# Kernel optimization log

Measured on AMD Instinct MI355X. Metric: run time of the kernel, lower is better.

## Reference

```python
import jax, jax.numpy as jnp
import numpy as np

N = 50000   # num nodes
E = 600000  # num edges (avg degree 12)
IN = 128
OUT = 128


def setup_inputs() -> dict:
    key = jax.random.key(0)
    ks = jax.random.split(key, 6)
    x = jax.random.normal(ks[0], (N, IN), dtype=jnp.float32)
    edge_index = jax.random.randint(ks[1], (2, E), 0, N, dtype=jnp.int32)
    # glorot-ish scaling for the linear weights
    W1 = jax.random.normal(ks[2], (IN, OUT), dtype=jnp.float32) / np.float32(np.sqrt(IN))
    b1 = jnp.zeros((OUT,), dtype=jnp.float32)
    W2 = jax.random.normal(ks[3], (OUT, OUT), dtype=jnp.float32) / np.float32(np.sqrt(OUT))
    b2 = jnp.zeros((OUT,), dtype=jnp.float32)
    return {"x": x, "edge_index": edge_index, "W1": W1, "b1": b1, "W2": W2, "b2": b2}


def gcn_conv(x, src, dst, W, b):
    # PyG GCNConv defaults: add self-loops, symmetric normalization D^-1/2 A D^-1/2.
    n = x.shape[0]
    deg = jax.ops.segment_sum(jnp.ones_like(dst, dtype=x.dtype), dst, num_segments=n)
    dinv = jnp.where(deg > 0, jax.lax.rsqrt(deg), 0.0)
    norm = dinv[src] * dinv[dst]            # [E+N]
    h = x @ W                               # [N, OUT]
    msg = h[src] * norm[:, None]            # gather + scale
    out = jax.ops.segment_sum(msg, dst, num_segments=n)  # scatter-add
    return out + b


def reference(x, edge_index, W1, b1, W2, b2):
    loop = jnp.arange(N, dtype=edge_index.dtype)
    src = jnp.concatenate([edge_index[0], loop])  # self-loops appended
    dst = jnp.concatenate([edge_index[1], loop])
    h = jax.nn.relu(gcn_conv(x, src, dst, W1, b1))
    out = jax.nn.relu(gcn_conv(h, src, dst, W2, b2))
    return out
```

## Files before the change

### kernel.cpp

```cpp
#include <hip/hip_runtime.h>
#include <hip/hip_bf16.h>


#define CAP 64

typedef short s16x8 __attribute__((ext_vector_type(8)));
typedef float f32x4 __attribute__((ext_vector_type(4)));

__device__ __forceinline__ unsigned short bf16_rne(float f) {
    unsigned u = __float_as_uint(f);
    return (unsigned short)((u + 0x7fffu + ((u >> 16) & 1u)) >> 16);
}


__global__ void setup_k(const float* __restrict__ W1, const float* __restrict__ W2,
                        short* __restrict__ wh1, short* __restrict__ wl1,
                        short* __restrict__ wh2, short* __restrict__ wl2,
                        int* __restrict__ cursor, int n) {
    int b = blockIdx.x;
    if (b >= 128) {
        int i = (b - 128) * 1024 + threadIdx.x * 4;
        if (i < n) {
            int4 z = make_int4(0, 0, 0, 0);
            if (i + 4 <= n) *(int4*)(cursor + i) = z;
            else for (int j = i; j < n; ++j) cursor[j] = 0;
        }
        return;
    }
    int gid = b * 256 + threadIdx.x;
    int which = gid >> 14;
    int tid = gid & 16383;
    const float* W = which ? W2 : W1;
    short* wh = which ? wh2 : wh1;
    short* wl = which ? wl2 : wl1;
    int k = tid >> 7, nn = tid & 127;
    float w = W[tid];
    unsigned u = __float_as_uint(w);
    unsigned hibits = (u + 0x7fffu + ((u >> 16) & 1u)) & 0xffff0000u;
    float rem = w - __uint_as_float(hibits);
    int kt = k >> 5, kr = k & 31, nt = nn >> 4, nr = nn & 15;
    int l = ((kr >> 3) << 4) | nr;
    int j = kr & 7;
    int dest = ((kt * 8 + nt) * 64 + l) * 8 + j;
    wh[dest] = (short)(hibits >> 16);
    wl[dest] = (short)bf16_rne(rem);
}

__global__ void fill_k(const int* __restrict__ src, const int* __restrict__ dst,
                       int* __restrict__ cursor, int* __restrict__ adj, int E) {
    int e = blockIdx.x * 256 + threadIdx.x;
    if (e < E) {
        int d = dst[e];
        int p = atomicAdd(&cursor[d], 1);
        if (p < CAP) adj[(size_t)d * CAP + p] = src[e];
    }
}

__device__ __forceinline__ void gemm_tile_compute(const char* lds,
                                                  const s16x8 BH[4][2], const s16x8 BL[4][2],
                                                  const int* __restrict__ cursor,
                                                  unsigned short* __restrict__ Hb,
                                                  int base, int n, int w, int rl, int kg) {
#pragma unroll
    for (int rt = 0; rt < 4; ++rt) {
        int row_local = rt * 16 + rl;
        int arow_byte = row_local * 256;
        int aswz = (row_local & 7) << 4;
        f32x4 acc[2] = {(f32x4){0.f,0.f,0.f,0.f}, (f32x4){0.f,0.f,0.f,0.f}};
#pragma unroll
        for (int kt = 0; kt < 4; ++kt) {
            int coff = (kt * 64 + (kg << 4)) ^ aswz;
            s16x8 ah = *(const s16x8*)(lds + arow_byte + coff);
#pragma unroll
            for (int i = 0; i < 2; ++i) {
                acc[i] = __builtin_amdgcn_mfma_f32_16x16x32_bf16(ah, BH[kt][i], acc[i], 0, 0, 0);
                acc[i] = __builtin_amdgcn_mfma_f32_16x16x32_bf16(ah, BL[kt][i], acc[i], 0, 0, 0);
            }
        }
        int r0 = base + rt * 16 + (kg << 2);
        float d0 = (r0 + 0 < n) ? rsqrtf((float)(cursor[r0 + 0] + 1)) : 0.f;
        float d1 = (r0 + 1 < n) ? rsqrtf((float)(cursor[r0 + 1] + 1)) : 0.f;
        float d2 = (r0 + 2 < n) ? rsqrtf((float)(cursor[r0 + 2] + 1)) : 0.f;
        float d3 = (r0 + 3 < n) ? rsqrtf((float)(cursor[r0 + 3] + 1)) : 0.f;
#pragma unroll
        for (int i = 0; i < 2; ++i) {
            int col = ((w * 2 + i) << 4) | rl;
            if (r0 + 0 < n) Hb[(size_t)(r0 + 0) * 128 + col] = bf16_rne(acc[i][0] * d0);
            if (r0 + 1 < n) Hb[(size_t)(r0 + 1) * 128 + col] = bf16_rne(acc[i][1] * d1);
            if (r0 + 2 < n) Hb[(size_t)(r0 + 2) * 128 + col] = bf16_rne(acc[i][2] * d2);
            if (r0 + 3 < n) Hb[(size_t)(r0 + 3) * 128 + col] = bf16_rne(acc[i][3] * d3);
        }
    }
}

__global__ __launch_bounds__(256) void gemm_mfma_f32(const float* __restrict__ X,
                                                     const short* __restrict__ wbh,
                                                     const short* __restrict__ wbl,
                                                     const int* __restrict__ cursor,
                                                     unsigned short* __restrict__ Hb,
                                                     int n) {
    __shared__ char lds[16384];
    int tid = threadIdx.x;
    int w = tid >> 6;
    int l = tid & 63;
    int rl = l & 15;
    int kg = l >> 4;
    int base = blockIdx.x * 64;

    const s16x8* bh8 = (const s16x8*)wbh;
    const s16x8* bl8 = (const s16x8*)wbl;
    s16x8 BH[4][2], BL[4][2];
#pragma unroll
    for (int kt = 0; kt < 4; ++kt)
#pragma unroll
        for (int i = 0; i < 2; ++i) {
            int f = kt * 8 + (w * 2 + i);
            BH[kt][i] = bh8[f * 64 + l];
            BL[kt][i] = bl8[f * 64 + l];
        }

#pragma unroll
    for (int u = 0; u < 4; ++u) {
        int idx = u * 256 + tid;
        int r = idx >> 4;
        int c0 = (idx & 15) * 8;
        int row = base + r;
        float v[8];
        if (row < n) {
            const float4* p = (const float4*)(X + (size_t)row * 128 + c0);
            float4 a = p[0], b = p[1];
            v[0]=a.x; v[1]=a.y; v[2]=a.z; v[3]=a.w;
            v[4]=b.x; v[5]=b.y; v[6]=b.z; v[7]=b.w;
        } else {
#pragma unroll
            for (int i = 0; i < 8; ++i) v[i] = 0.f;
        }
        short hi8[8];
#pragma unroll
        for (int i = 0; i < 8; ++i) hi8[i] = (short)bf16_rne(v[i]);
        int boff = r * 256 + ((c0 * 2) ^ ((r & 7) << 4));
        *(s16x8*)(lds + boff) = *(const s16x8*)hi8;
    }
    __syncthreads();
    gemm_tile_compute(lds, BH, BL, cursor, Hb, base, n, w, rl, kg);
}

__global__ __launch_bounds__(256) void gemm_mfma_bf16(const unsigned short* __restrict__ T,
                                                      const short* __restrict__ wbh,
                                                      const short* __restrict__ wbl,
                                                      const int* __restrict__ cursor,
                                                      unsigned short* __restrict__ Hb,
                                                      int n) {
    __shared__ char lds[16384];
    int tid = threadIdx.x;
    int w = tid >> 6;
    int l = tid & 63;
    int rl = l & 15;
    int kg = l >> 4;
    int base = blockIdx.x * 64;

    const s16x8* bh8 = (const s16x8*)wbh;
    const s16x8* bl8 = (const s16x8*)wbl;
    s16x8 BH[4][2], BL[4][2];
#pragma unroll
    for (int kt = 0; kt < 4; ++kt)
#pragma unroll
        for (int i = 0; i < 2; ++i) {
            int f = kt * 8 + (w * 2 + i);
            BH[kt][i] = bh8[f * 64 + l];
            BL[kt][i] = bl8[f * 64 + l];
        }

#pragma unroll
    for (int u = 0; u < 4; ++u) {
        int idx = u * 256 + tid;
        int r = idx >> 4;
        int cb = (idx & 15) * 16;
        int row = base + r;
        s16x8 val = {0,0,0,0,0,0,0,0};
        if (row < n) val = *(const s16x8*)(T + (size_t)row * 128 + cb / 2);
        int boff = r * 256 + (cb ^ ((r & 7) << 4));
        *(s16x8*)(lds + boff) = val;
    }
    __syncthreads();
    gemm_tile_compute(lds, BH, BL, cursor, Hb, base, n, w, rl, kg);
}


template <int SPLIT>
__global__ __launch_bounds__(256) void agg_k(const unsigned short* __restrict__ Hs,
                                             const int* __restrict__ cursor,
                                             const int* __restrict__ adj,
                                             const float* __restrict__ bias,
                                             float* __restrict__ fout,
                                             unsigned short* __restrict__ th,
                                             int n) {
    int node = blockIdx.x * 4 + (threadIdx.x >> 6);
    if (node >= n) return;
    node = __builtin_amdgcn_readfirstlane(node);
    int lane = threadIdx.x & 63;

    const unsigned* H1 = (const unsigned*)Hs;
    unsigned sraw = H1[(size_t)node * 64 + lane];
    float ax = __uint_as_float((sraw & 0xffffu) << 16);
    float ay = __uint_as_float(sraw & 0xffff0000u);

    int deg_raw = cursor[node];
    int e1 = deg_raw > CAP ? CAP : deg_raw;
    const int* alist = adj + (size_t)node * CAP;
    int e = 0;

    for (; e + 16 <= e1; e += 16) {
        int s[16];
#pragma unroll
        for (int i = 0; i < 16; ++i) s[i] = alist[e + i];
        unsigned rv[16];
#pragma unroll
        for (int i = 0; i < 16; ++i) rv[i] = H1[(size_t)s[i] * 64 + lane];
#pragma unroll
        for (int i = 0; i < 16; ++i) {
            ax += __uint_as_float((rv[i] & 0xffffu) << 16);
            ay += __uint_as_float(rv[i] & 0xffff0000u);
        }
    }
    for (; e + 4 <= e1; e += 4) {
        int s[4];
#pragma unroll
        for (int i = 0; i < 4; ++i) s[i] = alist[e + i];
        unsigned rv[4];
#pragma unroll
        for (int i = 0; i < 4; ++i) rv[i] = H1[(size_t)s[i] * 64 + lane];
#pragma unroll
        for (int i = 0; i < 4; ++i) {
            ax += __uint_as_float((rv[i] & 0xffffu) << 16);
            ay += __uint_as_float(rv[i] & 0xffff0000u);
        }
    }
    for (; e < e1; ++e) {
        unsigned rv = H1[(size_t)alist[e] * 64 + lane];
        ax += __uint_as_float((rv & 0xffffu) << 16);
        ay += __uint_as_float(rv & 0xffff0000u);
    }

    float di = rsqrtf((float)(deg_raw + 1));
    float2 b = ((const float2*)bias)[lane];
    float a0 = fmaxf(fmaf(ax, di, b.x), 0.f);
    float a1 = fmaxf(fmaf(ay, di, b.y), 0.f);
    if (SPLIT) {
        ((ushort2*)th)[(size_t)node * 64 + lane] = make_ushort2(bf16_rne(a0), bf16_rne(a1));
    } else {
        ((float2*)fout)[(size_t)node * 64 + lane] = make_float2(a0, a1);
    }
}


extern "C" void kernel_launch(void* const* d_in, const int* in_sizes, int n_in,
                              void* d_out, int out_size, void* d_ws, size_t ws_size,
                              hipStream_t stream) {
    const float* x  = (const float*)d_in[0];
    const int*   ei = (const int*)d_in[1];
    const float* W1 = (const float*)d_in[2];
    const float* b1 = (const float*)d_in[3];
    const float* W2 = (const float*)d_in[4];
    const float* b2 = (const float*)d_in[5];
    float* out = (float*)d_out;

    const int N = in_sizes[0] / 128;
    const int E = in_sizes[1] / 2;
    const int* src = ei;
    const int* dst = ei + E;

    char* ws = (char*)d_ws;
    size_t off = 0;
    auto alloc = [&](size_t bytes) -> void* {
        void* p = ws + off;
        off = (off + bytes + 255) & ~(size_t)255;
        return p;
    };
    int*   cursor  = (int*)  alloc((size_t)N * 4);
    int*   adj     = (int*)  alloc((size_t)N * CAP * 4);
    unsigned short* hb  = (unsigned short*)alloc((size_t)N * 128 * 2);
    unsigned short* th  = (unsigned short*)alloc((size_t)N * 128 * 2);
    unsigned short* hb2 = (unsigned short*)alloc((size_t)N * 128 * 2);
    short* w1h = (short*)alloc((size_t)128 * 128 * 2);
    short* w1l = (short*)alloc((size_t)128 * 128 * 2);
    short* w2h = (short*)alloc((size_t)128 * 128 * 2);
    short* w2l = (short*)alloc((size_t)128 * 128 * 2);
    (void)ws_size; (void)n_in; (void)out_size;

    int gE = (E + 255) / 256;
    int gA = (N + 3) / 4;
    int gG = (N + 63) / 64;
    int zb = (N + 1023) / 1024;

    setup_k<<<128 + zb, 256, 0, stream>>>(W1, W2, w1h, w1l, w2h, w2l, cursor, N);
    fill_k<<<gE, 256, 0, stream>>>(src, dst, cursor, adj, E);

    gemm_mfma_f32<<<gG, 256, 0, stream>>>(x, w1h, w1l, cursor, hb, N);
    agg_k<1><<<gA, 256, 0, stream>>>(hb, cursor, adj, b1, nullptr, th, N);
    gemm_mfma_bf16<<<gG, 256, 0, stream>>>(th, w2h, w2l, cursor, hb2, N);
    agg_k<0><<<gA, 256, 0, stream>>>(hb2, cursor, adj, b2, out, nullptr, N);
}
```

Baseline: 119.9 us.

## Fuse adjacency fill with first GEMM and move source normalization into aggregation

```diff
diff --git a/kernel.cpp b/kernel.cpp
--- a/kernel.cpp
+++ b/kernel.cpp
@@ -46,19 +46,8 @@
     wl[dest] = (short)bf16_rne(rem);
 }
 
-__global__ void fill_k(const int* __restrict__ src, const int* __restrict__ dst,
-                       int* __restrict__ cursor, int* __restrict__ adj, int E) {
-    int e = blockIdx.x * 256 + threadIdx.x;
-    if (e < E) {
-        int d = dst[e];
-        int p = atomicAdd(&cursor[d], 1);
-        if (p < CAP) adj[(size_t)d * CAP + p] = src[e];
-    }
-}
-
 __device__ __forceinline__ void gemm_tile_compute(const char* lds,
                                                   const s16x8 BH[4][2], const s16x8 BL[4][2],
-                                                  const int* __restrict__ cursor,
                                                   unsigned short* __restrict__ Hb,
                                                   int base, int n, int w, int rl, int kg) {
 #pragma unroll
@@ -78,46 +67,62 @@
             }
         }
         int r0 = base + rt * 16 + (kg << 2);
-        float d0 = (r0 + 0 < n) ? rsqrtf((float)(cursor[r0 + 0] + 1)) : 0.f;
-        float d1 = (r0 + 1 < n) ? rsqrtf((float)(cursor[r0 + 1] + 1)) : 0.f;
-        float d2 = (r0 + 2 < n) ? rsqrtf((float)(cursor[r0 + 2] + 1)) : 0.f;
-        float d3 = (r0 + 3 < n) ? rsqrtf((float)(cursor[r0 + 3] + 1)) : 0.f;
 #pragma unroll
         for (int i = 0; i < 2; ++i) {
             int col = ((w * 2 + i) << 4) | rl;
-            if (r0 + 0 < n) Hb[(size_t)(r0 + 0) * 128 + col] = bf16_rne(acc[i][0] * d0);
-            if (r0 + 1 < n) Hb[(size_t)(r0 + 1) * 128 + col] = bf16_rne(acc[i][1] * d1);
-            if (r0 + 2 < n) Hb[(size_t)(r0 + 2) * 128 + col] = bf16_rne(acc[i][2] * d2);
-            if (r0 + 3 < n) Hb[(size_t)(r0 + 3) * 128 + col] = bf16_rne(acc[i][3] * d3);
-        }
-    }
-}
-
-__global__ __launch_bounds__(256) void gemm_mfma_f32(const float* __restrict__ X,
-                                                     const short* __restrict__ wbh,
-                                                     const short* __restrict__ wbl,
-                                                     const int* __restrict__ cursor,
-                                                     unsigned short* __restrict__ Hb,
-                                                     int n) {
+            if (r0 + 0 < n) Hb[(size_t)(r0 + 0) * 128 + col] = bf16_rne(acc[i][0]);
+            if (r0 + 1 < n) Hb[(size_t)(r0 + 1) * 128 + col] = bf16_rne(acc[i][1]);
+            if (r0 + 2 < n) Hb[(size_t)(r0 + 2) * 128 + col] = bf16_rne(acc[i][2]);
+            if (r0 + 3 < n) Hb[(size_t)(r0 + 3) * 128 + col] = bf16_rne(acc[i][3]);
+        }
+    }
+}
+
+__device__ __forceinline__ void load_bfrags(const short* wbh, const short* wbl,
+                                            int w, int l, s16x8 BH[4][2], s16x8 BL[4][2]) {
+    const s16x8* bh8 = (const s16x8*)wbh;
+    const s16x8* bl8 = (const s16x8*)wbl;
+#pragma unroll
+    for (int kt = 0; kt < 4; ++kt)
+#pragma unroll
+        for (int i = 0; i < 2; ++i) {
+            int f = kt * 8 + (w * 2 + i);
+            BH[kt][i] = bh8[f * 64 + l];
+            BL[kt][i] = bl8[f * 64 + l];
+        }
+}
+
+__global__ __launch_bounds__(256) void fillgemm_k(const float* __restrict__ X,
+                                                  const short* __restrict__ wbh,
+                                                  const short* __restrict__ wbl,
+                                                  unsigned short* __restrict__ Hb,
+                                                  const int* __restrict__ src,
+                                                  const int* __restrict__ dst,
+                                                  int* __restrict__ cursor,
+                                                  int* __restrict__ adj,
+                                                  int n, int gG, int E) {
     __shared__ char lds[16384];
+    int b = blockIdx.x;
     int tid = threadIdx.x;
+
+    if (b >= gG) {
+        int e = (b - gG) * 256 + tid;
+        if (e < E) {
+            int d = dst[e];
+            int p = atomicAdd(&cursor[d], 1);
+            if (p < CAP) adj[(size_t)d * CAP + p] = src[e];
+        }
+        return;
+    }
+
     int w = tid >> 6;
     int l = tid & 63;
     int rl = l & 15;
     int kg = l >> 4;
-    int base = blockIdx.x * 64;
-
-    const s16x8* bh8 = (const s16x8*)wbh;
-    const s16x8* bl8 = (const s16x8*)wbl;
+    int base = b * 64;
+
     s16x8 BH[4][2], BL[4][2];
-#pragma unroll
-    for (int kt = 0; kt < 4; ++kt)
-#pragma unroll
-        for (int i = 0; i < 2; ++i) {
-            int f = kt * 8 + (w * 2 + i);
-            BH[kt][i] = bh8[f * 64 + l];
-            BL[kt][i] = bl8[f * 64 + l];
-        }
+    load_bfrags(wbh, wbl, w, l, BH, BL);
 
 #pragma unroll
     for (int u = 0; u < 4; ++u) {
@@ -128,9 +133,9 @@
         float v[8];
         if (row < n) {
             const float4* p = (const float4*)(X + (size_t)row * 128 + c0);
-            float4 a = p[0], b = p[1];
+            float4 a = p[0], bb = p[1];
             v[0]=a.x; v[1]=a.y; v[2]=a.z; v[3]=a.w;
-            v[4]=b.x; v[5]=b.y; v[6]=b.z; v[7]=b.w;
+            v[4]=bb.x; v[5]=bb.y; v[6]=bb.z; v[7]=bb.w;
         } else {
 #pragma unroll
             for (int i = 0; i < 8; ++i) v[i] = 0.f;
@@ -142,13 +147,12 @@
         *(s16x8*)(lds + boff) = *(const s16x8*)hi8;
     }
     __syncthreads();
-    gemm_tile_compute(lds, BH, BL, cursor, Hb, base, n, w, rl, kg);
+    gemm_tile_compute(lds, BH, BL, Hb, base, n, w, rl, kg);
 }
 
 __global__ __launch_bounds__(256) void gemm_mfma_bf16(const unsigned short* __restrict__ T,
                                                       const short* __restrict__ wbh,
                                                       const short* __restrict__ wbl,
-                                                      const int* __restrict__ cursor,
                                                       unsigned short* __restrict__ Hb,
                                                       int n) {
     __shared__ char lds[16384];
@@ -159,17 +163,8 @@
     int kg = l >> 4;
     int base = blockIdx.x * 64;
 
-    const s16x8* bh8 = (const s16x8*)wbh;
-    const s16x8* bl8 = (const s16x8*)wbl;
     s16x8 BH[4][2], BL[4][2];
-#pragma unroll
-    for (int kt = 0; kt < 4; ++kt)
-#pragma unroll
-        for (int i = 0; i < 2; ++i) {
-            int f = kt * 8 + (w * 2 + i);
-            BH[kt][i] = bh8[f * 64 + l];
-            BL[kt][i] = bl8[f * 64 + l];
-        }
+    load_bfrags(wbh, wbl, w, l, BH, BL);
 
 #pragma unroll
     for (int u = 0; u < 4; ++u) {
@@ -183,7 +178,7 @@
         *(s16x8*)(lds + boff) = val;
     }
     __syncthreads();
-    gemm_tile_compute(lds, BH, BL, cursor, Hb, base, n, w, rl, kg);
+    gemm_tile_compute(lds, BH, BL, Hb, base, n, w, rl, kg);
 }
 
 
@@ -201,11 +196,13 @@
     int lane = threadIdx.x & 63;
 
     const unsigned* H1 = (const unsigned*)Hs;
+    int deg_raw = cursor[node];
+    float di = rsqrtf((float)(deg_raw + 1));
+
     unsigned sraw = H1[(size_t)node * 64 + lane];
-    float ax = __uint_as_float((sraw & 0xffffu) << 16);
-    float ay = __uint_as_float(sraw & 0xffff0000u);
-
-    int deg_raw = cursor[node];
+    float ax = __uint_as_float((sraw & 0xffffu) << 16) * di;
+    float ay = __uint_as_float(sraw & 0xffff0000u) * di;
+
     int e1 = deg_raw > CAP ? CAP : deg_raw;
     const int* alist = adj + (size_t)node * CAP;
     int e = 0;
@@ -214,35 +211,42 @@
         int s[16];
 #pragma unroll
         for (int i = 0; i < 16; ++i) s[i] = alist[e + i];
+        float ww[16];
+#pragma unroll
+        for (int i = 0; i < 16; ++i) ww[i] = rsqrtf((float)(cursor[s[i]] + 1));
         unsigned rv[16];
 #pragma unroll
         for (int i = 0; i < 16; ++i) rv[i] = H1[(size_t)s[i] * 64 + lane];
 #pragma unroll
         for (int i = 0; i < 16; ++i) {
-            ax += __uint_as_float((rv[i] & 0xffffu) << 16);
-            ay += __uint_as_float(rv[i] & 0xffff0000u);
+            ax = fmaf(__uint_as_float((rv[i] & 0xffffu) << 16), ww[i], ax);
+            ay = fmaf(__uint_as_float(rv[i] & 0xffff0000u), ww[i], ay);
         }
     }
     for (; e + 4 <= e1; e += 4) {
         int s[4];
 #pragma unroll
         for (int i = 0; i < 4; ++i) s[i] = alist[e + i];
+        float ww[4];
+#pragma unroll
+        for (int i = 0; i < 4; ++i) ww[i] = rsqrtf((float)(cursor[s[i]] + 1));
         unsigned rv[4];
 #pragma unroll
         for (int i = 0; i < 4; ++i) rv[i] = H1[(size_t)s[i] * 64 + lane];
 #pragma unroll
         for (int i = 0; i < 4; ++i) {
-            ax += __uint_as_float((rv[i] & 0xffffu) << 16);
-            ay += __uint_as_float(rv[i] & 0xffff0000u);
+            ax = fmaf(__uint_as_float((rv[i] & 0xffffu) << 16), ww[i], ax);
+            ay = fmaf(__uint_as_float(rv[i] & 0xffff0000u), ww[i], ay);
         }
     }
     for (; e < e1; ++e) {
-        unsigned rv = H1[(size_t)alist[e] * 64 + lane];
-        ax += __uint_as_float((rv & 0xffffu) << 16);
-        ay += __uint_as_float(rv & 0xffff0000u);
-    }
-
-    float di = rsqrtf((float)(deg_raw + 1));
+        int s = alist[e];
+        float wwe = rsqrtf((float)(cursor[s] + 1));
+        unsigned rv = H1[(size_t)s * 64 + lane];
+        ax = fmaf(__uint_as_float((rv & 0xffffu) << 16), wwe, ax);
+        ay = fmaf(__uint_as_float(rv & 0xffff0000u), wwe, ay);
+    }
+
     float2 b = ((const float2*)bias)[lane];
     float a0 = fmaxf(fmaf(ax, di, b.x), 0.f);
     float a1 = fmaxf(fmaf(ay, di, b.y), 0.f);
@@ -294,10 +298,9 @@
     int zb = (N + 1023) / 1024;
 
     setup_k<<<128 + zb, 256, 0, stream>>>(W1, W2, w1h, w1l, w2h, w2l, cursor, N);
-    fill_k<<<gE, 256, 0, stream>>>(src, dst, cursor, adj, E);
-
-    gemm_mfma_f32<<<gG, 256, 0, stream>>>(x, w1h, w1l, cursor, hb, N);
+    fillgemm_k<<<gG + gE, 256, 0, stream>>>(x, w1h, w1l, hb, src, dst, cursor, adj,
+                                            N, gG, E);
     agg_k<1><<<gA, 256, 0, stream>>>(hb, cursor, adj, b1, nullptr, th, N);
-    gemm_mfma_bf16<<<gG, 256, 0, stream>>>(th, w2h, w2l, cursor, hb2, N);
+    gemm_mfma_bf16<<<gG, 256, 0, stream>>>(th, w2h, w2l, hb2, N);
     agg_k<0><<<gA, 256, 0, stream>>>(hb2, cursor, adj, b2, out, nullptr, N);
 }
```

Result: slower. 152.1 us (+26.8%).
